# Performance work log

Hardware: AMD Instinct MI355X
Metric: run time of the kernel (lower is better)

Reference implementation:

```python
import jax, jax.numpy as jnp
import numpy as np

MB, E, N, IN_HALF, HID, OUT = 32, 4, 512, 64, 128, 128
EPS = 1e-5


def setup_inputs() -> dict:
    key = jax.random.key(0)
    ks = jax.random.split(key, 24)
    x = jax.random.normal(ks[0], (MB, N, IN_HALF), jnp.float32)
    u = jax.random.uniform(ks[1], (MB, E, N, N), jnp.float32)
    a = (u < 0.02).astype(jnp.float32)
    adj = jnp.maximum(a, jnp.swapaxes(a, -1, -2))  # symmetric 0/1, forward's sym branch holds
    def lin(k, i, o):
        return jax.random.normal(k, (i, o), jnp.float32) / np.float32(np.sqrt(i))
    d = {"x": x, "adj": adj}
    in_dims = [IN_HALF, HID, HID]
    for l in range(3):
        d[f"w_self{l}"] = lin(ks[2 + 6 * l], in_dims[l], HID)
        d[f"b_self{l}"] = jnp.zeros((HID,), jnp.float32)
        d[f"w_edge{l}"] = lin(ks[3 + 6 * l], in_dims[l], HID * E)
        d[f"b_edge{l}"] = jnp.zeros((HID * E,), jnp.float32)
        d[f"bn{l}_g"] = jnp.ones((N,), jnp.float32)
        d[f"bn{l}_b"] = jnp.zeros((N,), jnp.float32)
    d["w1"] = lin(ks[20], HID, HID)
    d["b1"] = jnp.zeros((HID,), jnp.float32)
    d["bn_f_g"] = jnp.ones((N,), jnp.float32)
    d["bn_f_b"] = jnp.zeros((N,), jnp.float32)
    d["w2"] = lin(ks[21], HID, OUT)
    d["b2"] = jnp.zeros((OUT,), jnp.float32)
    return d


def _rescale_adj(adj):
    # zero the diagonal, then normalize each column by total neighbor count
    n = adj.shape[-1]
    adj = adj * (1.0 - jnp.eye(n, dtype=adj.dtype))
    deg = adj.sum(axis=(1, 2))  # (mb, N): sum over edge types and rows
    inv = jnp.where(deg > 0, 1.0 / deg, 0.0)
    return inv[:, None, None, :] * adj


def _batchnorm_nodes(h, g, b):
    # torch BatchNorm1d(n_node) on (B, N, D): per-node stats over (B, D), biased var
    m = h.mean(axis=(0, 2), keepdims=True)
    v = ((h - m) ** 2).mean(axis=(0, 2), keepdims=True)
    return (h - m) / jnp.sqrt(v + EPS) * g[None, :, None] + b[None, :, None]


def _graph_conv(h, na, w_self, b_self, w_edge, b_edge):
    mb, n, _ = h.shape
    hs = h @ w_self + b_self  # (mb, N, out)
    m = (h @ w_edge + b_edge).reshape(mb, n, HID, E)  # (mb, N, out, E)
    # fused: per-edge-type adj matmul + sum over edge types, no (mb,E,N,out) blowup
    hr = jnp.einsum('benm,bmoe->bno', na, m)
    return hs + hr


def reference(x, adj,
              w_self0, b_self0, w_edge0, b_edge0, bn0_g, bn0_b,
              w_self1, b_self1, w_edge1, b_edge1, bn1_g, bn1_b,
              w_self2, b_self2, w_edge2, b_edge2, bn2_g, bn2_b,
              w1, b1, bn_f_g, bn_f_b, w2, b2):
    # adj is symmetric by construction -> forward's adj_sym == adj
    na = _rescale_adj(adj)  # identical across layers; computed once
    h = x
    layers = [
        (w_self0, b_self0, w_edge0, b_edge0, bn0_g, bn0_b),
        (w_self1, b_self1, w_edge1, b_edge1, bn1_g, bn1_b),
        (w_self2, b_self2, w_edge2, b_edge2, bn2_g, bn2_b),
    ]
    for ws, bs, we, be, g, b in layers:
        h = _graph_conv(h, na, ws, bs, we, be)
        h = _batchnorm_nodes(h, g, b)
        h = jax.nn.relu(h)
    h = h @ w1 + b1
    h = _batchnorm_nodes(h, bn_f_g, bn_f_b)
    h = jax.nn.relu(h)
    h = h @ w2 + b2
    return h
```

## Files before the change

kernel.cpp:

```cpp
#include <hip/hip_runtime.h>
#include <stdint.h>


typedef float  f32x4  __attribute__((ext_vector_type(4)));
typedef __bf16 bf16x8 __attribute__((ext_vector_type(8)));
typedef __bf16 bf16x4 __attribute__((ext_vector_type(4)));
typedef unsigned short ushort8v __attribute__((ext_vector_type(8)));
typedef uint32_t uint4v __attribute__((ext_vector_type(4)));

#define MBATCH 32
#define ETYPES 4
#define NNODE  512
#define HIDD   128

#define GLB(p) (const __attribute__((address_space(1))) uint32_t*)(p)
#define LDSp(p) (__attribute__((address_space(3))) uint32_t*)(p)

#define WP_S0 0
#define WP_E0 8192
#define WP_S1 40960
#define WP_E1 57344
#define WP_S2 122880
#define WP_E2 139264
#define WP_W1 204800
#define WP_W2 221184
#define WP_TOT 237568

__global__ __launch_bounds__(256) void k_pack(const float* __restrict__ adj,
                                              uint32_t* __restrict__ bm,
                                              float* __restrict__ deg) {
  int t = threadIdx.x;
  int wave = t >> 6, lane = t & 63;
  int r = blockIdx.x * 4 + wave;
  int b = r >> 11, n = r & 511;
  const float* row = adj + (long)r * 512;
  uint32_t myw = 0;
#pragma unroll
  for (int i = 0; i < 8; ++i) {
    uint64_t bal = __ballot(row[i * 64 + lane] != 0.f);
    uint32_t lo = (uint32_t)bal, hi = (uint32_t)(bal >> 32);
    if ((lane >> 1) == i) myw = (lane & 1) ? hi : lo;
  }
  if (lane == (n >> 5)) myw &= ~(1u << (n & 31));
  int pc = (lane < 16) ? __popc(myw) : 0;
  pc += __shfl_down(pc, 8);
  pc += __shfl_down(pc, 4);
  pc += __shfl_down(pc, 2);
  pc += __shfl_down(pc, 1);
  if (lane < 16) bm[(long)r * 16 + lane] = myw;
  if (lane == 0) atomicAdd(&deg[b * 512 + n], (float)pc);
}

__global__ __launch_bounds__(256) void k_inv(const float* __restrict__ deg,
                                             float* __restrict__ inv) {
  int i = blockIdx.x * 256 + threadIdx.x;
  float d = deg[i];
  inv[i] = d > 0.f ? 1.f / d : 0.f;
}

__global__ __launch_bounds__(256) void k_cast(const float* __restrict__ in,
                                              __bf16* __restrict__ out) {
  int i = blockIdx.x * 256 + threadIdx.x;
  f32x4 v = *(const f32x4*)(in + (long)i * 4);
  bf16x4 o;
#pragma unroll
  for (int j = 0; j < 4; ++j) o[j] = (__bf16)v[j];
  *(bf16x4*)(out + (long)i * 4) = o;
}

__global__ __launch_bounds__(256) void k_prep(const float* ws0, const float* we0,
                                              const float* ws1, const float* we1,
                                              const float* ws2, const float* we2,
                                              const float* w1,  const float* w2,
                                              __bf16* __restrict__ dst) {
  int wid = blockIdx.y;
  const float* W; int K, nblk, edge, off;
  switch (wid) {
    case 0:  W = ws0; K = 64;  nblk = 2; edge = 0; off = WP_S0; break;
    case 1:  W = we0; K = 64;  nblk = 8; edge = 1; off = WP_E0; break;
    case 2:  W = ws1; K = 128; nblk = 2; edge = 0; off = WP_S1; break;
    case 3:  W = we1; K = 128; nblk = 8; edge = 1; off = WP_E1; break;
    case 4:  W = ws2; K = 128; nblk = 2; edge = 0; off = WP_S2; break;
    case 5:  W = we2; K = 128; nblk = 8; edge = 1; off = WP_E2; break;
    case 6:  W = w1;  K = 128; nblk = 2; edge = 0; off = WP_W1; break;
    default: W = w2;  K = 128; nblk = 2; edge = 0; off = WP_W2; break;
  }
  int idx = blockIdx.x * 256 + threadIdx.x;
  if (idx >= K * nblk * 64) return;
  int c = idx & 63;
  int k = (idx >> 6) % K;
  int blk = (idx >> 6) / K;
  int WS = edge ? 512 : 128;
  int col = edge ? (((blk & 1) * 64 + c) * 4 + (blk >> 1)) : (blk * 64 + c);
  dst[off + (long)blk * K * 64 + (k >> 3) * 512 + c * 8 + (k & 7)] = (__bf16)W[k * WS + col];
}

template <int K>
__global__ __launch_bounds__(256) void k_gemm(const __bf16* __restrict__ h,
                                              const __bf16* __restrict__ wp_self,
                                              const float* __restrict__ bias_self,
                                              const __bf16* __restrict__ wp_edge,
                                              const float* __restrict__ bias_edge,
                                              const float* __restrict__ invp,
                                              float* __restrict__ outF,
                                              __bf16* __restrict__ mmp) {
  __shared__ __bf16 Hl[64][K + 8];
  __shared__ __align__(16) __bf16 Wl[K * 64];
  int t = threadIdx.x;
  int g0 = blockIdx.x * 64;
  int by = blockIdx.y;
  bool edge = by >= 2;
  int wave = t >> 6, lane = t & 63;
  {
    const __bf16* wblk = edge ? (wp_edge + (long)(by - 2) * K * 64)
                              : (wp_self + (long)by * K * 64);
    const char* g = (const char*)wblk;
#pragma unroll
    for (int i = 0; i < K / 32; ++i) {
      __builtin_amdgcn_global_load_lds(GLB(g + i * 4096 + wave * 1024 + lane * 16),
                                       LDSp((char*)Wl + i * 4096 + wave * 1024),
                                       16, 0, 0);
    }
  }
  for (int idx = t; idx < 64 * (K / 8); idx += 256) {
    int r = idx / (K / 8), ch = idx % (K / 8);
    *(bf16x8*)&Hl[r][ch * 8] = *(const bf16x8*)(h + (long)(g0 + r) * K + ch * 8);
  }
  __syncthreads();
  int l15 = lane & 15, q = lane >> 4;
  f32x4 acc[4] = {};
#pragma unroll
  for (int kk = 0; kk < K / 32; ++kk) {
    bf16x8 af = *(const bf16x8*)&Hl[wave * 16 + l15][kk * 32 + q * 8];
#pragma unroll
    for (int c = 0; c < 4; ++c) {
      bf16x8 bfr = *(const bf16x8*)&Wl[((kk * 4 + q) * 64 + c * 16 + l15) * 8];
      acc[c] = __builtin_amdgcn_mfma_f32_16x16x32_bf16(af, bfr, acc[c], 0, 0, 0);
    }
  }
  if (!edge) {
    int c0 = by * 64;
#pragma unroll
    for (int c = 0; c < 4; ++c) {
      float bc = bias_self[c0 + c * 16 + l15];
#pragma unroll
      for (int i = 0; i < 4; ++i) {
        int g = g0 + wave * 16 + q * 4 + i;
        outF[(long)g * HIDD + c0 + c * 16 + l15] = acc[c][i] + bc;
      }
    }
  } else {
    int blk = by - 2;
    int e = blk >> 1, o0 = (blk & 1) * 64;
    float iv[4];
#pragma unroll
    for (int i = 0; i < 4; ++i) iv[i] = invp[g0 + wave * 16 + q * 4 + i];
    int b4e  = (g0 >> 9) * 4 + e;
    int octg = ((g0 & 511) >> 3) + wave * 2 + (q >> 1);
    int j0   = (q & 1) * 4;
#pragma unroll
    for (int c = 0; c < 4; ++c) {
      int o = o0 + c * 16 + l15;
      float bc = bias_edge[o * 4 + e];
      bf16x4 v4;
#pragma unroll
      for (int i = 0; i < 4; ++i) v4[i] = (__bf16)((acc[c][i] + bc) * iv[i]);
      *(bf16x4*)(mmp + ((long)(b4e * 64 + octg) * HIDD + o) * 8 + j0) = v4;
    }
  }
}

__global__ __launch_bounds__(256) void k_spmm(const uint32_t* __restrict__ bm,
                                              const __bf16* __restrict__ mmp,
                                              float* __restrict__ part) {
  __shared__ __align__(16) __bf16 Bl[8192];
  int t = threadIdx.x;
  int bid = blockIdx.x;
  int e = bid >> 7, b = (bid >> 2) & 31, nt = bid & 3;
  int n0 = nt * 128;
  int wave = t >> 6, lane = t & 63, l15 = lane & 15, q = lane >> 4;

  const uint32_t* bmr0 = bm + ((long)((b * 4 + e) * 512 + n0 + wave * 32 + l15)) * 16;
  uint32_t rm0[16], rm1[16];
#pragma unroll
  for (int i = 0; i < 4; ++i) {
    uint4v v0 = *(const uint4v*)(bmr0 + i * 4);
    uint4v v1 = *(const uint4v*)(bmr0 + 256 + i * 4);
    rm0[i * 4 + 0] = v0.x; rm0[i * 4 + 1] = v0.y; rm0[i * 4 + 2] = v0.z; rm0[i * 4 + 3] = v0.w;
    rm1[i * 4 + 0] = v1.x; rm1[i * 4 + 1] = v1.y; rm1[i * 4 + 2] = v1.z; rm1[i * 4 + 3] = v1.w;
  }

  const __bf16* Bbase = mmp + (long)(b * 4 + e) * 65536;
  f32x4 acc0[8] = {}, acc1[8] = {};
#pragma unroll 1
  for (int mc = 0; mc < 8; ++mc) {
    __syncthreads();
    const char* g = (const char*)(Bbase + mc * 8192);
#pragma unroll
    for (int i = 0; i < 4; ++i) {
      __builtin_amdgcn_global_load_lds(GLB(g + i * 4096 + wave * 1024 + lane * 16),
                                       LDSp((char*)Bl + i * 4096 + wave * 1024),
                                       16, 0, 0);
    }
    __syncthreads();
#pragma unroll
    for (int kk = 0; kk < 2; ++kk) {
      uint32_t bits0 = (rm0[mc * 2 + kk] >> (q * 8)) & 0xffu;
      uint32_t bits1 = (rm1[mc * 2 + kk] >> (q * 8)) & 0xffu;
      ushort8v a0, a1;
#pragma unroll
      for (int j = 0; j < 8; ++j) {
        a0[j] = (bits0 >> j & 1u) ? (unsigned short)0x3F80 : (unsigned short)0;
        a1[j] = (bits1 >> j & 1u) ? (unsigned short)0x3F80 : (unsigned short)0;
      }
      union { ushort8v u; bf16x8 v; } c0, c1; c0.u = a0; c1.u = a1;
#pragma unroll
      for (int c = 0; c < 8; ++c) {
        bf16x8 bfr = *(const bf16x8*)&Bl[(kk * 4 + q) * 1024 + (c * 16 + l15) * 8];
        acc0[c] = __builtin_amdgcn_mfma_f32_16x16x32_bf16(c0.v, bfr, acc0[c], 0, 0, 0);
        acc1[c] = __builtin_amdgcn_mfma_f32_16x16x32_bf16(c1.v, bfr, acc1[c], 0, 0, 0);
      }
    }
  }
  float* dst = part + (long)(e * 32 + b) * NNODE * HIDD;
#pragma unroll
  for (int c = 0; c < 8; ++c) {
#pragma unroll
    for (int i = 0; i < 4; ++i) {
      int n = n0 + wave * 32 + q * 4 + i;
      int o = c * 16 + l15;
      dst[(long)n * HIDD + o] = acc0[c][i];
      dst[(long)(n + 16) * HIDD + o] = acc1[c][i];
    }
  }
}

template <bool HASP>
__global__ __launch_bounds__(256) void k_bnstat(const float* __restrict__ hs,
                                                const float* __restrict__ part,
                                                const float* __restrict__ gg,
                                                const float* __restrict__ bb,
                                                __bf16* __restrict__ hb) {
  int n = blockIdx.x, t = threadIdx.x;
  int o4 = t & 31, bq = t >> 5;
  __shared__ float sm[4096];
  __shared__ float rs[256], rq[256];
  __shared__ float bc[2];
  float s = 0.f, sq = 0.f;
#pragma unroll
  for (int i = 0; i < 4; ++i) {
    int b = bq + i * 8;
    long base = ((long)b * NNODE + n) * HIDD + o4 * 4;
    f32x4 v = *(const f32x4*)(hs + base);
    if (HASP) {
#pragma unroll
      for (int e = 0; e < 4; ++e)
        v += *(const f32x4*)(part + ((long)(e * 32 + b) * NNODE + n) * HIDD + o4 * 4);
    }
    *(f32x4*)&sm[b * 128 + o4 * 4] = v;
#pragma unroll
    for (int j = 0; j < 4; ++j) { s += v[j]; sq += v[j] * v[j]; }
  }
  rs[t] = s; rq[t] = sq;
  __syncthreads();
  for (int off = 128; off > 0; off >>= 1) {
    if (t < off) { rs[t] += rs[t + off]; rq[t] += rq[t + off]; }
    __syncthreads();
  }
  if (t == 0) {
    float mean = rs[0] * (1.f / 4096.f);
    float var = rq[0] * (1.f / 4096.f) - mean * mean;
    float rstd = rsqrtf(var + 1e-5f);
    float sc = gg[n] * rstd;
    bc[0] = sc;
    bc[1] = bb[n] - mean * sc;
  }
  __syncthreads();
  float sc = bc[0], sh = bc[1];
#pragma unroll
  for (int i = 0; i < 4; ++i) {
    int b = bq + i * 8;
    f32x4 v = *(const f32x4*)&sm[b * 128 + o4 * 4];
    bf16x4 o;
#pragma unroll
    for (int j = 0; j < 4; ++j) {
      float x = v[j] * sc + sh;
      o[j] = (__bf16)(x > 0.f ? x : 0.f);
    }
    *(bf16x4*)(hb + ((long)b * NNODE + n) * HIDD + o4 * 4) = o;
  }
}

extern "C" void kernel_launch(void* const* d_in, const int* in_sizes, int n_in,
                              void* d_out, int out_size, void* d_ws, size_t ws_size,
                              hipStream_t stream) {
  (void)in_sizes; (void)n_in; (void)out_size; (void)ws_size;
  const float* x   = (const float*)d_in[0];
  const float* adj = (const float*)d_in[1];
  const float* wself[3] = {(const float*)d_in[2],  (const float*)d_in[8],  (const float*)d_in[14]};
  const float* bself[3] = {(const float*)d_in[3],  (const float*)d_in[9],  (const float*)d_in[15]};
  const float* wedge[3] = {(const float*)d_in[4],  (const float*)d_in[10], (const float*)d_in[16]};
  const float* bedge[3] = {(const float*)d_in[5],  (const float*)d_in[11], (const float*)d_in[17]};
  const float* bng[3]   = {(const float*)d_in[6],  (const float*)d_in[12], (const float*)d_in[18]};
  const float* bnb[3]   = {(const float*)d_in[7],  (const float*)d_in[13], (const float*)d_in[19]};
  const float* w1   = (const float*)d_in[20];
  const float* b1   = (const float*)d_in[21];
  const float* bnfg = (const float*)d_in[22];
  const float* bnfb = (const float*)d_in[23];
  const float* w2   = (const float*)d_in[24];
  const float* b2   = (const float*)d_in[25];

  char* ws = (char*)d_ws;
  __bf16*   mmp  = (__bf16*)ws;
  float*    hs   = (float*)(ws + 16777216);
  float*    part = (float*)(ws + 25165824);
  __bf16*   hb0  = (__bf16*)(ws + 58720256);
  __bf16*   hb1  = (__bf16*)(ws + 62914560);
  __bf16*   xb   = (__bf16*)(ws + 67108864);
  uint32_t* bm   = (uint32_t*)(ws + 69206016);
  float*    deg  = (float*)(ws + 73400320);
  float*    inv  = (float*)(ws + 73465856);
  __bf16*   wp   = (__bf16*)(ws + 73531392);

  hipMemsetAsync(deg, 0, MBATCH * NNODE * sizeof(float), stream);
  k_cast<<<1024, 256, 0, stream>>>(x, xb);
  k_pack<<<16384, 256, 0, stream>>>(adj, bm, deg);
  k_inv<<<64, 256, 0, stream>>>(deg, inv);
  k_prep<<<dim3(256, 8), 256, 0, stream>>>(wself[0], wedge[0], wself[1], wedge[1],
                                           wself[2], wedge[2], w1, w2, wp);

  k_gemm<64><<<dim3(256, 10), 256, 0, stream>>>(xb, wp + WP_S0, bself[0], wp + WP_E0,
                                                bedge[0], inv, hs, mmp);
  k_spmm<<<512, 256, 0, stream>>>(bm, mmp, part);
  k_bnstat<true><<<512, 256, 0, stream>>>(hs, part, bng[0], bnb[0], hb0);

  k_gemm<128><<<dim3(256, 10), 256, 0, stream>>>(hb0, wp + WP_S1, bself[1], wp + WP_E1,
                                                 bedge[1], inv, hs, mmp);
  k_spmm<<<512, 256, 0, stream>>>(bm, mmp, part);
  k_bnstat<true><<<512, 256, 0, stream>>>(hs, part, bng[1], bnb[1], hb1);

  k_gemm<128><<<dim3(256, 10), 256, 0, stream>>>(hb1, wp + WP_S2, bself[2], wp + WP_E2,
                                                 bedge[2], inv, hs, mmp);
  k_spmm<<<512, 256, 0, stream>>>(bm, mmp, part);
  k_bnstat<true><<<512, 256, 0, stream>>>(hs, part, bng[2], bnb[2], hb0);

  k_gemm<128><<<dim3(256, 2), 256, 0, stream>>>(hb0, wp + WP_W1, b1, nullptr,
                                                nullptr, nullptr, hs, nullptr);
  k_bnstat<false><<<512, 256, 0, stream>>>(hs, nullptr, bnfg, bnfb, hb1);
  k_gemm<128><<<dim3(256, 2), 256, 0, stream>>>(hb1, wp + WP_W2, b2, nullptr,
                                                nullptr, nullptr, (float*)d_out, nullptr);
}
```

Before: 372.7 us.

## Accumulate edge-type sum inside spmm and fold cast and degree atomics away

The sparse aggregation kernel now loops over all four edge types inside one block, which tiles over output columns (64 at a time), and adds its result straight into the self-term buffer with read-modify-write. This removes the 32 MB per-edge partial buffer and its re-read in the batchnorm kernel. The input fp32-to-bf16 cast is fused into the first GEMM's tile load, and degree counting writes per-edge partials instead of using atomics and a memset. In exchange, spmm launches only 256 blocks, so parallelism is lower, and adjacency bitmasks are reloaded for each column tile.

```diff
diff --git a/kernel.cpp b/kernel.cpp
--- a/kernel.cpp
+++ b/kernel.cpp
@@ -24,15 +24,14 @@
 #define WP_E2 139264
 #define WP_W1 204800
 #define WP_W2 221184
-#define WP_TOT 237568
 
 __global__ __launch_bounds__(256) void k_pack(const float* __restrict__ adj,
                                               uint32_t* __restrict__ bm,
-                                              float* __restrict__ deg) {
+                                              float* __restrict__ degp) {
   int t = threadIdx.x;
   int wave = t >> 6, lane = t & 63;
   int r = blockIdx.x * 4 + wave;
-  int b = r >> 11, n = r & 511;
+  int b = r >> 11, e = (r >> 9) & 3, n = r & 511;
   const float* row = adj + (long)r * 512;
   uint32_t myw = 0;
 #pragma unroll
@@ -48,24 +47,14 @@
   pc += __shfl_down(pc, 2);
   pc += __shfl_down(pc, 1);
   if (lane < 16) bm[(long)r * 16 + lane] = myw;
-  if (lane == 0) atomicAdd(&deg[b * 512 + n], (float)pc);
-}
-
-__global__ __launch_bounds__(256) void k_inv(const float* __restrict__ deg,
+  if (lane == 0) degp[e * 16384 + b * 512 + n] = (float)pc;
+}
+
+__global__ __launch_bounds__(256) void k_inv(const float* __restrict__ degp,
                                              float* __restrict__ inv) {
   int i = blockIdx.x * 256 + threadIdx.x;
-  float d = deg[i];
+  float d = degp[i] + degp[16384 + i] + degp[32768 + i] + degp[49152 + i];
   inv[i] = d > 0.f ? 1.f / d : 0.f;
-}
-
-__global__ __launch_bounds__(256) void k_cast(const float* __restrict__ in,
-                                              __bf16* __restrict__ out) {
-  int i = blockIdx.x * 256 + threadIdx.x;
-  f32x4 v = *(const f32x4*)(in + (long)i * 4);
-  bf16x4 o;
-#pragma unroll
-  for (int j = 0; j < 4; ++j) o[j] = (__bf16)v[j];
-  *(bf16x4*)(out + (long)i * 4) = o;
 }
 
 __global__ __launch_bounds__(256) void k_prep(const float* ws0, const float* we0,
@@ -95,8 +84,8 @@
   dst[off + (long)blk * K * 64 + (k >> 3) * 512 + c * 8 + (k & 7)] = (__bf16)W[k * WS + col];
 }
 
-template <int K>
-__global__ __launch_bounds__(256) void k_gemm(const __bf16* __restrict__ h,
+template <int K, bool F32IN>
+__global__ __launch_bounds__(256) void k_gemm(const void* __restrict__ hv,
                                               const __bf16* __restrict__ wp_self,
                                               const float* __restrict__ bias_self,
                                               const __bf16* __restrict__ wp_edge,
@@ -124,7 +113,18 @@
   }
   for (int idx = t; idx < 64 * (K / 8); idx += 256) {
     int r = idx / (K / 8), ch = idx % (K / 8);
-    *(bf16x8*)&Hl[r][ch * 8] = *(const bf16x8*)(h + (long)(g0 + r) * K + ch * 8);
+    if (F32IN) {
+      const float* xf = (const float*)hv;
+      f32x4 a = *(const f32x4*)(xf + (long)(g0 + r) * K + ch * 8);
+      f32x4 bq = *(const f32x4*)(xf + (long)(g0 + r) * K + ch * 8 + 4);
+      bf16x8 o;
+#pragma unroll
+      for (int j = 0; j < 4; ++j) { o[j] = (__bf16)a[j]; o[4 + j] = (__bf16)bq[j]; }
+      *(bf16x8*)&Hl[r][ch * 8] = o;
+    } else {
+      const __bf16* hb = (const __bf16*)hv;
+      *(bf16x8*)&Hl[r][ch * 8] = *(const bf16x8*)(hb + (long)(g0 + r) * K + ch * 8);
+    }
   }
   __syncthreads();
   int l15 = lane & 15, q = lane >> 4;
@@ -172,72 +172,74 @@
 
 __global__ __launch_bounds__(256) void k_spmm(const uint32_t* __restrict__ bm,
                                               const __bf16* __restrict__ mmp,
-                                              float* __restrict__ part) {
-  __shared__ __align__(16) __bf16 Bl[8192];
+                                              float* __restrict__ hs) {
+  __shared__ __align__(16) __bf16 Bl[4096];
   int t = threadIdx.x;
   int bid = blockIdx.x;
-  int e = bid >> 7, b = (bid >> 2) & 31, nt = bid & 3;
-  int n0 = nt * 128;
+  int b = bid & 31, nt = (bid >> 5) & 3, oc = bid >> 7;
+  int n0 = nt * 128, o0 = oc * 64;
   int wave = t >> 6, lane = t & 63, l15 = lane & 15, q = lane >> 4;
 
-  const uint32_t* bmr0 = bm + ((long)((b * 4 + e) * 512 + n0 + wave * 32 + l15)) * 16;
-  uint32_t rm0[16], rm1[16];
-#pragma unroll
-  for (int i = 0; i < 4; ++i) {
-    uint4v v0 = *(const uint4v*)(bmr0 + i * 4);
-    uint4v v1 = *(const uint4v*)(bmr0 + 256 + i * 4);
-    rm0[i * 4 + 0] = v0.x; rm0[i * 4 + 1] = v0.y; rm0[i * 4 + 2] = v0.z; rm0[i * 4 + 3] = v0.w;
-    rm1[i * 4 + 0] = v1.x; rm1[i * 4 + 1] = v1.y; rm1[i * 4 + 2] = v1.z; rm1[i * 4 + 3] = v1.w;
-  }
-
-  const __bf16* Bbase = mmp + (long)(b * 4 + e) * 65536;
-  f32x4 acc0[8] = {}, acc1[8] = {};
+  f32x4 acc0[4] = {}, acc1[4] = {};
+  for (int e = 0; e < 4; ++e) {
+    const uint32_t* bmr = bm + ((long)((b * 4 + e) * 512 + n0 + wave * 32 + l15)) * 16;
+    uint32_t rm0[16], rm1[16];
+#pragma unroll
+    for (int i = 0; i < 4; ++i) {
+      uint4v v0 = *(const uint4v*)(bmr + i * 4);
+      uint4v v1 = *(const uint4v*)(bmr + 256 + i * 4);
+      rm0[i * 4 + 0] = v0.x; rm0[i * 4 + 1] = v0.y; rm0[i * 4 + 2] = v0.z; rm0[i * 4 + 3] = v0.w;
+      rm1[i * 4 + 0] = v1.x; rm1[i * 4 + 1] = v1.y; rm1[i * 4 + 2] = v1.z; rm1[i * 4 + 3] = v1.w;
+    }
+    const __bf16* Bbase = mmp + (long)(b * 4 + e) * 65536;
 #pragma unroll 1
-  for (int mc = 0; mc < 8; ++mc) {
+    for (int mc = 0; mc < 8; ++mc) {
+      __syncthreads();
+#pragma unroll
+      for (int i = 0; i < 2; ++i) {
+        int oct = wave * 2 + i;
+        const char* g = (const char*)mmp +
+            ((long)(b * 4 + e) * 65536 + mc * 8192 + oct * 1024 + o0 * 8) * 2;
+        __builtin_amdgcn_global_load_lds(GLB(g + lane * 16),
+                                         LDSp((char*)Bl + oct * 1024),
+                                         16, 0, 0);
+      }
+      __syncthreads();
+#pragma unroll
+      for (int kk = 0; kk < 2; ++kk) {
+        uint32_t bits0 = (rm0[mc * 2 + kk] >> (q * 8)) & 0xffu;
+        uint32_t bits1 = (rm1[mc * 2 + kk] >> (q * 8)) & 0xffu;
+        ushort8v a0, a1;
+#pragma unroll
+        for (int j = 0; j < 8; ++j) {
+          a0[j] = (bits0 >> j & 1u) ? (unsigned short)0x3F80 : (unsigned short)0;
+          a1[j] = (bits1 >> j & 1u) ? (unsigned short)0x3F80 : (unsigned short)0;
+        }
+        union { ushort8v u; bf16x8 v; } c0, c1; c0.u = a0; c1.u = a1;
+#pragma unroll
+        for (int c = 0; c < 4; ++c) {
+          bf16x8 bfr = *(const bf16x8*)&Bl[((kk * 4 + q) * 64 + c * 16 + l15) * 8];
+          acc0[c] = __builtin_amdgcn_mfma_f32_16x16x32_bf16(c0.v, bfr, acc0[c], 0, 0, 0);
+          acc1[c] = __builtin_amdgcn_mfma_f32_16x16x32_bf16(c1.v, bfr, acc1[c], 0, 0, 0);
+        }
+      }
+    }
     __syncthreads();
-    const char* g = (const char*)(Bbase + mc * 8192);
-#pragma unroll
-    for (int i = 0; i < 4; ++i) {
-      __builtin_amdgcn_global_load_lds(GLB(g + i * 4096 + wave * 1024 + lane * 16),
-                                       LDSp((char*)Bl + i * 4096 + wave * 1024),
-                                       16, 0, 0);
-    }
-    __syncthreads();
-#pragma unroll
-    for (int kk = 0; kk < 2; ++kk) {
-      uint32_t bits0 = (rm0[mc * 2 + kk] >> (q * 8)) & 0xffu;
-      uint32_t bits1 = (rm1[mc * 2 + kk] >> (q * 8)) & 0xffu;
-      ushort8v a0, a1;
-#pragma unroll
-      for (int j = 0; j < 8; ++j) {
-        a0[j] = (bits0 >> j & 1u) ? (unsigned short)0x3F80 : (unsigned short)0;
-        a1[j] = (bits1 >> j & 1u) ? (unsigned short)0x3F80 : (unsigned short)0;
-      }
-      union { ushort8v u; bf16x8 v; } c0, c1; c0.u = a0; c1.u = a1;
-#pragma unroll
-      for (int c = 0; c < 8; ++c) {
-        bf16x8 bfr = *(const bf16x8*)&Bl[(kk * 4 + q) * 1024 + (c * 16 + l15) * 8];
-        acc0[c] = __builtin_amdgcn_mfma_f32_16x16x32_bf16(c0.v, bfr, acc0[c], 0, 0, 0);
-        acc1[c] = __builtin_amdgcn_mfma_f32_16x16x32_bf16(c1.v, bfr, acc1[c], 0, 0, 0);
-      }
-    }
-  }
-  float* dst = part + (long)(e * 32 + b) * NNODE * HIDD;
-#pragma unroll
-  for (int c = 0; c < 8; ++c) {
+  }
+#pragma unroll
+  for (int c = 0; c < 4; ++c) {
 #pragma unroll
     for (int i = 0; i < 4; ++i) {
       int n = n0 + wave * 32 + q * 4 + i;
-      int o = c * 16 + l15;
-      dst[(long)n * HIDD + o] = acc0[c][i];
-      dst[(long)(n + 16) * HIDD + o] = acc1[c][i];
-    }
-  }
-}
-
-template <bool HASP>
+      int o = o0 + c * 16 + l15;
+      long idx = ((long)b * NNODE + n) * HIDD + o;
+      hs[idx] += acc0[c][i];
+      hs[idx + 16 * HIDD] += acc1[c][i];
+    }
+  }
+}
+
 __global__ __launch_bounds__(256) void k_bnstat(const float* __restrict__ hs,
-                                                const float* __restrict__ part,
                                                 const float* __restrict__ gg,
                                                 const float* __restrict__ bb,
                                                 __bf16* __restrict__ hb) {
@@ -250,13 +252,7 @@
 #pragma unroll
   for (int i = 0; i < 4; ++i) {
     int b = bq + i * 8;
-    long base = ((long)b * NNODE + n) * HIDD + o4 * 4;
-    f32x4 v = *(const f32x4*)(hs + base);
-    if (HASP) {
-#pragma unroll
-      for (int e = 0; e < 4; ++e)
-        v += *(const f32x4*)(part + ((long)(e * 32 + b) * NNODE + n) * HIDD + o4 * 4);
-    }
+    f32x4 v = *(const f32x4*)(hs + ((long)b * NNODE + n) * HIDD + o4 * 4);
     *(f32x4*)&sm[b * 128 + o4 * 4] = v;
 #pragma unroll
     for (int j = 0; j < 4; ++j) { s += v[j]; sq += v[j] * v[j]; }
@@ -313,40 +309,36 @@
   char* ws = (char*)d_ws;
   __bf16*   mmp  = (__bf16*)ws;
   float*    hs   = (float*)(ws + 16777216);
-  float*    part = (float*)(ws + 25165824);
-  __bf16*   hb0  = (__bf16*)(ws + 58720256);
-  __bf16*   hb1  = (__bf16*)(ws + 62914560);
-  __bf16*   xb   = (__bf16*)(ws + 67108864);
-  uint32_t* bm   = (uint32_t*)(ws + 69206016);
-  float*    deg  = (float*)(ws + 73400320);
-  float*    inv  = (float*)(ws + 73465856);
-  __bf16*   wp   = (__bf16*)(ws + 73531392);
-
-  hipMemsetAsync(deg, 0, MBATCH * NNODE * sizeof(float), stream);
-  k_cast<<<1024, 256, 0, stream>>>(x, xb);
-  k_pack<<<16384, 256, 0, stream>>>(adj, bm, deg);
-  k_inv<<<64, 256, 0, stream>>>(deg, inv);
+  __bf16*   hb0  = (__bf16*)(ws + 25165824);
+  __bf16*   hb1  = (__bf16*)(ws + 29360128);
+  uint32_t* bm   = (uint32_t*)(ws + 33554432);
+  float*    degp = (float*)(ws + 37748736);
+  float*    inv  = (float*)(ws + 38010880);
+  __bf16*   wp   = (__bf16*)(ws + 38076416);
+
+  k_pack<<<16384, 256, 0, stream>>>(adj, bm, degp);
+  k_inv<<<64, 256, 0, stream>>>(degp, inv);
   k_prep<<<dim3(256, 8), 256, 0, stream>>>(wself[0], wedge[0], wself[1], wedge[1],
                                            wself[2], wedge[2], w1, w2, wp);
 
-  k_gemm<64><<<dim3(256, 10), 256, 0, stream>>>(xb, wp + WP_S0, bself[0], wp + WP_E0,
-                                                bedge[0], inv, hs, mmp);
-  k_spmm<<<512, 256, 0, stream>>>(bm, mmp, part);
-  k_bnstat<true><<<512, 256, 0, stream>>>(hs, part, bng[0], bnb[0], hb0);
-
-  k_gemm<128><<<dim3(256, 10), 256, 0, stream>>>(hb0, wp + WP_S1, bself[1], wp + WP_E1,
-                                                 bedge[1], inv, hs, mmp);
-  k_spmm<<<512, 256, 0, stream>>>(bm, mmp, part);
-  k_bnstat<true><<<512, 256, 0, stream>>>(hs, part, bng[1], bnb[1], hb1);
-
-  k_gemm<128><<<dim3(256, 10), 256, 0, stream>>>(hb1, wp + WP_S2, bself[2], wp + WP_E2,
-                                                 bedge[2], inv, hs, mmp);
-  k_spmm<<<512, 256, 0, stream>>>(bm, mmp, part);
-  k_bnstat<true><<<512, 256, 0, stream>>>(hs, part, bng[2], bnb[2], hb0);
-
-  k_gemm<128><<<dim3(256, 2), 256, 0, stream>>>(hb0, wp + WP_W1, b1, nullptr,
-                                                nullptr, nullptr, hs, nullptr);
-  k_bnstat<false><<<512, 256, 0, stream>>>(hs, nullptr, bnfg, bnfb, hb1);
-  k_gemm<128><<<dim3(256, 2), 256, 0, stream>>>(hb1, wp + WP_W2, b2, nullptr,
-                                                nullptr, nullptr, (float*)d_out, nullptr);
-}
+  k_gemm<64, true><<<dim3(256, 10), 256, 0, stream>>>(x, wp + WP_S0, bself[0], wp + WP_E0,
+                                                      bedge[0], inv, hs, mmp);
+  k_spmm<<<256, 256, 0, stream>>>(bm, mmp, hs);
+  k_bnstat<<<512, 256, 0, stream>>>(hs, bng[0], bnb[0], hb0);
+
+  k_gemm<128, false><<<dim3(256, 10), 256, 0, stream>>>(hb0, wp + WP_S1, bself[1], wp + WP_E1,
+                                                        bedge[1], inv, hs, mmp);
+  k_spmm<<<256, 256, 0, stream>>>(bm, mmp, hs);
+  k_bnstat<<<512, 256, 0, stream>>>(hs, bng[1], bnb[1], hb1);
+
+  k_gemm<128, false><<<dim3(256, 10), 256, 0, stream>>>(hb1, wp + WP_S2, bself[2], wp + WP_E2,
+                                                        bedge[2], inv, hs, mmp);
+  k_spmm<<<256, 256, 0, stream>>>(bm, mmp, hs);
+  k_bnstat<<<512, 256, 0, stream>>>(hs, bng[2], bnb[2], hb0);
+
+  k_gemm<128, false><<<dim3(256, 2), 256, 0, stream>>>(hb0, wp + WP_W1, b1, nullptr,
+                                                       nullptr, nullptr, hs, nullptr);
+  k_bnstat<<<512, 256, 0, stream>>>(hs, bnfg, bnfb, hb1);
+  k_gemm<128, false><<<dim3(256, 2), 256, 0, stream>>>(hb1, wp + WP_W2, b2, nullptr,
+                                                       nullptr, nullptr, (float*)d_out, nullptr);
+}
```

Result: slower. 413.4 us (+10.9%).
